# Kernel optimization log

Measured on AMD Instinct MI355X. Metric: run time of the kernel, lower is better.

Reference implementation:

```python
import jax, jax.numpy as jnp
import numpy as np

N = 1024
B = 128
DT = 0.1
STEPS = 10

def setup_inputs() -> dict:
    key = jax.random.key(0)
    k1, k2, k3 = jax.random.split(key, 3)
    theta_init = jax.random.normal(k1, (B, N), dtype=jnp.float32)
    K0 = jax.random.normal(k2, (N, N), dtype=jnp.float32) * 0.1
    K = (K0 + K0.T) / 2  # symmetric coupling matrix, as in __init__
    omega = jax.random.normal(k3, (N,), dtype=jnp.float32) * 0.1
    K_global = jnp.asarray(0.5, dtype=jnp.float32)
    return {"theta_init": theta_init, "K": K, "omega": omega, "K_global": K_global}

def _compute_coherence(theta):
    # Kuramoto order parameter r = |<e^{i theta}>| over oscillator axis
    cos_mean = jnp.cos(theta).mean(axis=-1)
    sin_mean = jnp.sin(theta).mean(axis=-1)
    return jnp.sqrt(cos_mean ** 2 + sin_mean ** 2)

def reference(theta_init, K, omega, K_global):
    n = theta_init.shape[-1]

    def step(theta, _):
        # theta_diff[b, i, j] = theta[b, j] - theta[b, i]
        theta_diff = theta[..., None, :] - theta[..., :, None]  # [B, n, n]
        coupling_sum = (K * jnp.sin(theta_diff)).sum(axis=-1)   # [B, n]
        dtheta = omega + (K_global / n) * coupling_sum
        theta_new = theta + DT * dtheta
        # wrap to (-pi, pi]
        theta_new = jnp.arctan2(jnp.sin(theta_new), jnp.cos(theta_new))
        return theta_new, None

    theta, _ = jax.lax.scan(step, theta_init, None, length=STEPS)
    coherence = _compute_coherence(theta)
    return theta, coherence
```

## Files before the change

kernel.cpp:

```cpp
#include <hip/hip_runtime.h>
#include <math.h>

#define KN 1024
#define KB 128
#define KDT 0.1f
#define KSTEPS 10
#define KMAGIC 0xB0000000u
#define PI_F 3.14159265358979f
#define TWO_PI_F 6.28318530717959f

typedef __attribute__((ext_vector_type(8))) short short8;
typedef __attribute__((ext_vector_type(4))) float floatx4;
typedef unsigned long long u64;

__device__ __forceinline__ unsigned short f2bf(float f) {
    unsigned u = __float_as_uint(f);
    u += 0x7FFF + ((u >> 16) & 1);
    return (unsigned short)(u >> 16);
}

__device__ __forceinline__ unsigned xidx(int grp, int b15, int k) {
    return (unsigned)(grp * 16384 + (k >> 5) * 512 + ((k >> 1) & 3) * 128 +
                      ((k >> 3) & 3) * 32 + b15 * 2 + (k & 1));
}

__global__ __launch_bounds__(512)
void k_main(const float* __restrict__ theta0,
            const float* __restrict__ Kmat,
            const float* __restrict__ omega,
            const float* __restrict__ kg,
            float* __restrict__ out_theta,
            float* __restrict__ out_coh,
            unsigned* __restrict__ flags,
            float* __restrict__ acc,
            unsigned* __restrict__ xbuf)
{
    const int grp = blockIdx.x >> 5;
    const int b0  = grp * 16;
    const int i0  = (blockIdx.x & 31) * 32;

    const int tid  = threadIdx.x;
    const int lane = tid & 63;
    const int kq   = tid >> 6;
    const int r16  = lane & 15;
    const int quad = lane >> 4;

    __shared__ float ldsY[8][2][16][34];

    if ((blockIdx.x & 31) == 0 && tid < 16) {
        __hip_atomic_store(&acc[(b0 + tid) * 16], 0.f, __ATOMIC_RELAXED,
                           __HIP_MEMORY_SCOPE_AGENT);
        __hip_atomic_store(&acc[2048 + (b0 + tid) * 16], 0.f, __ATOMIC_RELAXED,
                           __HIP_MEMORY_SCOPE_AGENT);
    }

    short8 bfrag[2][4];
    #pragma unroll
    for (int wi = 0; wi < 2; ++wi) {
        const float* kp = Kmat + (size_t)(i0 + wi * 16 + r16) * KN + kq * 128 + quad * 8;
        #pragma unroll
        for (int it = 0; it < 4; ++it) {
            const float4 v0 = *reinterpret_cast<const float4*>(kp + it * 32);
            const float4 v1 = *reinterpret_cast<const float4*>(kp + it * 32 + 4);
            short8 b_;
            b_[0] = (short)f2bf(v0.x); b_[1] = (short)f2bf(v0.y);
            b_[2] = (short)f2bf(v0.z); b_[3] = (short)f2bf(v0.w);
            b_[4] = (short)f2bf(v1.x); b_[5] = (short)f2bf(v1.y);
            b_[6] = (short)f2bf(v1.z); b_[7] = (short)f2bf(v1.w);
            bfrag[wi][it] = b_;
        }
    }

    const int eb = b0 + (tid >> 5);
    const int ei = i0 + (tid & 31);
    float th_reg = theta0[(size_t)eb * KN + ei];
    const float omg = omega[ei];
    float sn, cs;
    __sincosf(th_reg, &sn, &cs);
    unsigned* xb[3] = {xbuf, xbuf + (size_t)KB * KN, xbuf + 2 * (size_t)KB * KN};
    const unsigned xoff = xidx(grp, eb & 15, ei);
    __hip_atomic_store(&xb[0][xoff],
                       (unsigned)f2bf(sn) | ((unsigned)f2bf(cs) << 16),
                       __ATOMIC_RELAXED, __HIP_MEMORY_SCOPE_AGENT);
    const float scale = kg[0] * (1.0f / (float)KN);

    __syncthreads();
    if (tid == 0)
        __hip_atomic_store(&flags[blockIdx.x], KMAGIC + 0u,
                           __ATOMIC_RELAXED, __HIP_MEMORY_SCOPE_AGENT);

    auto wait_chunks = [&](unsigned tgt) {
        unsigned polls = 0;
        for (;;) {
            unsigned v = tgt;
            if (lane < 4)
                v = __hip_atomic_load(&flags[grp * 32 + kq * 4 + lane],
                                      __ATOMIC_RELAXED, __HIP_MEMORY_SCOPE_AGENT);
            if (__ballot(v >= tgt) == ~0ull) break;
            if (++polls > 4000000u) break;
            __builtin_amdgcn_s_sleep(1);
        }
        asm volatile("" ::: "memory");
    };

    float s2 = sn, c2 = cs;
    for (int s = 0; s < KSTEPS; ++s) {
        wait_chunks(KMAGIC + (unsigned)s);

        const u64* xg = (const u64*)xb[s % 3] + grp * 8192 + kq * 1024 + lane;
        u64 aw[4][4];
        #pragma unroll
        for (int it = 0; it < 4; ++it)
            #pragma unroll
            for (int jj = 0; jj < 4; ++jj)
                aw[it][jj] = __hip_atomic_load((u64*)(xg + it * 256 + jj * 64),
                                               __ATOMIC_RELAXED,
                                               __HIP_MEMORY_SCOPE_AGENT);
        floatx4 accS[2] = {{0.f,0.f,0.f,0.f},{0.f,0.f,0.f,0.f}};
        floatx4 accC[2] = {{0.f,0.f,0.f,0.f},{0.f,0.f,0.f,0.f}};
        #pragma unroll
        for (int it = 0; it < 4; ++it) {
            short8 a_s, a_c;
            #pragma unroll
            for (int jj = 0; jj < 4; ++jj) {
                unsigned lo = (unsigned)aw[it][jj];
                unsigned hi = (unsigned)(aw[it][jj] >> 32);
                a_s[jj * 2]     = (short)(lo & 0xffffu);
                a_c[jj * 2]     = (short)(lo >> 16);
                a_s[jj * 2 + 1] = (short)(hi & 0xffffu);
                a_c[jj * 2 + 1] = (short)(hi >> 16);
            }
            #pragma unroll
            for (int wi = 0; wi < 2; ++wi) {
                accS[wi] = __builtin_amdgcn_mfma_f32_16x16x32_bf16(a_s, bfrag[wi][it], accS[wi], 0, 0, 0);
                accC[wi] = __builtin_amdgcn_mfma_f32_16x16x32_bf16(a_c, bfrag[wi][it], accC[wi], 0, 0, 0);
            }
        }
        #pragma unroll
        for (int wi = 0; wi < 2; ++wi)
            #pragma unroll
            for (int r = 0; r < 4; ++r) {
                ldsY[kq][0][quad * 4 + r][wi * 16 + r16] = accS[wi][r];
                ldsY[kq][1][quad * 4 + r][wi * 16 + r16] = accC[wi][r];
            }
        __syncthreads();

        {
            const int bl = tid >> 5, ilo = tid & 31;
            float Ys = 0.f, Yc = 0.f;
            #pragma unroll
            for (int q = 0; q < 8; ++q) {
                Ys += ldsY[q][0][bl][ilo];
                Yc += ldsY[q][1][bl][ilo];
            }
            const float coupling = cs * Ys - sn * Yc;
            float tn = th_reg + KDT * (omg + scale * coupling);
            __sincosf(tn, &s2, &c2);
            if (tn > PI_F)       tn -= TWO_PI_F;
            else if (tn < -PI_F) tn += TWO_PI_F;
            th_reg = tn;
            sn = s2; cs = c2;
        }
        if (s < KSTEPS - 1) {
            __hip_atomic_store(&xb[(s + 1) % 3][xoff],
                               (unsigned)f2bf(s2) | ((unsigned)f2bf(c2) << 16),
                               __ATOMIC_RELAXED, __HIP_MEMORY_SCOPE_AGENT);
            __syncthreads();
            if (tid == 0)
                __hip_atomic_store(&flags[blockIdx.x], KMAGIC + (unsigned)(s + 1),
                                   __ATOMIC_RELAXED, __HIP_MEMORY_SCOPE_AGENT);
        } else {
            out_theta[(size_t)eb * KN + ei] = th_reg;
        }
    }

    __syncthreads();
    float* red = &ldsY[0][0][0][0];
    red[tid]       = s2;
    red[512 + tid] = c2;
    __syncthreads();
    if (tid < 16) {
        float ss = 0.f, cc = 0.f;
        #pragma unroll
        for (int il2 = 0; il2 < 32; ++il2) {
            ss += red[tid * 32 + il2];
            cc += red[512 + tid * 32 + il2];
        }
        atomicAdd(&acc[(b0 + tid) * 16], ss);
        atomicAdd(&acc[2048 + (b0 + tid) * 16], cc);
    }
    __syncthreads();
    if (tid == 0)
        __hip_atomic_store(&flags[blockIdx.x], KMAGIC + (unsigned)KSTEPS,
                           __ATOMIC_RELAXED, __HIP_MEMORY_SCOPE_AGENT);

    if ((blockIdx.x & 31) == 0) {
        if (tid < 64) {
            const unsigned tgt = KMAGIC + (unsigned)KSTEPS;
            unsigned polls = 0;
            for (;;) {
                unsigned v = tgt;
                if (lane < 32)
                    v = __hip_atomic_load(&flags[grp * 32 + lane],
                                          __ATOMIC_RELAXED, __HIP_MEMORY_SCOPE_AGENT);
                if (__ballot(v >= tgt) == ~0ull) break;
                if (++polls > 4000000u) break;
                __builtin_amdgcn_s_sleep(2);
            }
        }
        asm volatile("" ::: "memory");
        __syncthreads();
        if (tid < 16) {
            float sv = __hip_atomic_load(&acc[(b0 + tid) * 16],
                                         __ATOMIC_RELAXED, __HIP_MEMORY_SCOPE_AGENT);
            float cv = __hip_atomic_load(&acc[2048 + (b0 + tid) * 16],
                                         __ATOMIC_RELAXED, __HIP_MEMORY_SCOPE_AGENT);
            float sm = sv * (1.0f / (float)KN);
            float cm = cv * (1.0f / (float)KN);
            out_coh[b0 + tid] = sqrtf(cm * cm + sm * sm);
        }
    }
}

extern "C" void kernel_launch(void* const* d_in, const int* in_sizes, int n_in,
                              void* d_out, int out_size, void* d_ws, size_t ws_size,
                              hipStream_t stream)
{
    (void)in_sizes; (void)n_in; (void)out_size; (void)ws_size;

    const float* theta0 = (const float*)d_in[0];
    const float* Kmat   = (const float*)d_in[1];
    const float* omega  = (const float*)d_in[2];
    const float* kg     = (const float*)d_in[3];

    float* out_theta = (float*)d_out;
    float* out_coh   = out_theta + (size_t)KB * KN;

    unsigned* flags = (unsigned*)d_ws;
    float* acc      = (float*)((char*)d_ws + 4096);
    unsigned* xbuf  = (unsigned*)((char*)d_ws + 32768);

    k_main<<<256, 512, 0, stream>>>(theta0, Kmat, omega, kg,
                                    out_theta, out_coh, flags, acc, xbuf);
}
```

Baseline: 98.02 us.

## Tag exchange buffer entries with epoch to skip flag polling

Each sin/cos exchange entry becomes a 64-bit word that carries an epoch tag in its upper half. Readers load the data first and check the tags, and only fall back to polling the per-block flags when some entry is stale. The aim is to remove flag-wait latency from the critical path between steps. The cost is twice the memory traffic for the exchange buffer. It also relies on 64-bit atomic stores being seen whole, and the epoch encoding (11 for the last step) has to avoid collisions with stale data left from earlier launches.

```diff
diff --git a/kernel.cpp b/kernel.cpp
--- a/kernel.cpp
+++ b/kernel.cpp
@@ -19,9 +19,9 @@
     return (unsigned short)(u >> 16);
 }
 
-__device__ __forceinline__ unsigned xidx(int grp, int b15, int k) {
-    return (unsigned)(grp * 16384 + (k >> 5) * 512 + ((k >> 1) & 3) * 128 +
-                      ((k >> 3) & 3) * 32 + b15 * 2 + (k & 1));
+__device__ __forceinline__ unsigned xoff64(int grp, int b15, int k) {
+    return (unsigned)(grp * 16384 + (k >> 5) * 512 + (k & 7) * 64 +
+                      ((k >> 3) & 3) * 16 + b15);
 }
 
 __global__ __launch_bounds__(512)
@@ -33,7 +33,7 @@
             float* __restrict__ out_coh,
             unsigned* __restrict__ flags,
             float* __restrict__ acc,
-            unsigned* __restrict__ xbuf)
+            u64* __restrict__ xbuf)
 {
     const int grp = blockIdx.x >> 5;
     const int b0  = grp * 16;
@@ -77,10 +77,11 @@
     const float omg = omega[ei];
     float sn, cs;
     __sincosf(th_reg, &sn, &cs);
-    unsigned* xb[3] = {xbuf, xbuf + (size_t)KB * KN, xbuf + 2 * (size_t)KB * KN};
-    const unsigned xoff = xidx(grp, eb & 15, ei);
+    u64* xb[3] = {xbuf, xbuf + (size_t)KB * KN, xbuf + 2 * (size_t)KB * KN};
+    const unsigned xoff = xoff64(grp, eb & 15, ei);
     __hip_atomic_store(&xb[0][xoff],
-                       (unsigned)f2bf(sn) | ((unsigned)f2bf(cs) << 16),
+                       (u64)((unsigned)f2bf(sn) | ((unsigned)f2bf(cs) << 16)) |
+                           (1ull << 32),
                        __ATOMIC_RELAXED, __HIP_MEMORY_SCOPE_AGENT);
     const float scale = kg[0] * (1.0f / (float)KN);
 
@@ -105,30 +106,46 @@
 
     float s2 = sn, c2 = cs;
     for (int s = 0; s < KSTEPS; ++s) {
-        wait_chunks(KMAGIC + (unsigned)s);
-
-        const u64* xg = (const u64*)xb[s % 3] + grp * 8192 + kq * 1024 + lane;
-        u64 aw[4][4];
+        const unsigned es = (s == 9) ? 11u : (unsigned)(s + 1);
+
+        const u64* xg = xb[s % 3] + grp * 16384 + kq * 2048 + lane;
+        u64 aw[4][8];
         #pragma unroll
         for (int it = 0; it < 4; ++it)
             #pragma unroll
-            for (int jj = 0; jj < 4; ++jj)
-                aw[it][jj] = __hip_atomic_load((u64*)(xg + it * 256 + jj * 64),
-                                               __ATOMIC_RELAXED,
-                                               __HIP_MEMORY_SCOPE_AGENT);
+            for (int h = 0; h < 8; ++h)
+                aw[it][h] = __hip_atomic_load(xg + it * 512 + h * 64,
+                                              __ATOMIC_RELAXED,
+                                              __HIP_MEMORY_SCOPE_AGENT);
+        {
+            int ok = 1;
+            #pragma unroll
+            for (int it = 0; it < 4; ++it)
+                #pragma unroll
+                for (int h = 0; h < 8; ++h)
+                    ok &= ((unsigned)(aw[it][h] >> 32) == es);
+            if (__ballot(ok != 0) != ~0ull) {
+                wait_chunks(KMAGIC + (unsigned)s);
+                #pragma unroll
+                for (int it = 0; it < 4; ++it)
+                    #pragma unroll
+                    for (int h = 0; h < 8; ++h)
+                        aw[it][h] = __hip_atomic_load(xg + it * 512 + h * 64,
+                                                      __ATOMIC_RELAXED,
+                                                      __HIP_MEMORY_SCOPE_AGENT);
+            }
+        }
+
         floatx4 accS[2] = {{0.f,0.f,0.f,0.f},{0.f,0.f,0.f,0.f}};
         floatx4 accC[2] = {{0.f,0.f,0.f,0.f},{0.f,0.f,0.f,0.f}};
         #pragma unroll
         for (int it = 0; it < 4; ++it) {
             short8 a_s, a_c;
             #pragma unroll
-            for (int jj = 0; jj < 4; ++jj) {
-                unsigned lo = (unsigned)aw[it][jj];
-                unsigned hi = (unsigned)(aw[it][jj] >> 32);
-                a_s[jj * 2]     = (short)(lo & 0xffffu);
-                a_c[jj * 2]     = (short)(lo >> 16);
-                a_s[jj * 2 + 1] = (short)(hi & 0xffffu);
-                a_c[jj * 2 + 1] = (short)(hi >> 16);
+            for (int h = 0; h < 8; ++h) {
+                const unsigned lo = (unsigned)aw[it][h];
+                a_s[h] = (short)(lo & 0xffffu);
+                a_c[h] = (short)(lo >> 16);
             }
             #pragma unroll
             for (int wi = 0; wi < 2; ++wi) {
@@ -162,8 +179,10 @@
             sn = s2; cs = c2;
         }
         if (s < KSTEPS - 1) {
+            const unsigned e1 = (s == 8) ? 11u : (unsigned)(s + 2);
             __hip_atomic_store(&xb[(s + 1) % 3][xoff],
-                               (unsigned)f2bf(s2) | ((unsigned)f2bf(c2) << 16),
+                               (u64)((unsigned)f2bf(s2) | ((unsigned)f2bf(c2) << 16)) |
+                                   ((u64)e1 << 32),
                                __ATOMIC_RELAXED, __HIP_MEMORY_SCOPE_AGENT);
             __syncthreads();
             if (tid == 0)
@@ -238,7 +257,7 @@
 
     unsigned* flags = (unsigned*)d_ws;
     float* acc      = (float*)((char*)d_ws + 4096);
-    unsigned* xbuf  = (unsigned*)((char*)d_ws + 32768);
+    u64* xbuf       = (u64*)((char*)d_ws + 32768);
 
     k_main<<<256, 512, 0, stream>>>(theta0, Kmat, omega, kg,
                                     out_theta, out_coh, flags, acc, xbuf);
```

After: 122.5 us. 24.9% more time.
